# Kernel optimization log

Hardware: AMD Instinct MI355X
Metric: run time of the kernel (lower is better)

Reference implementation:

```python
import jax, jax.numpy as jnp
import numpy as np

EPS = 1e-10
WS = 5  # window_size
PAD = WS // 2


def _conv(x, k, pad_h, pad_w):
    # x: [N,1,H,W], k: [1,1,kh,kw], 'same'-style explicit padding
    return jax.lax.conv_general_dilated(
        x, k, window_strides=(1, 1),
        padding=[(pad_h, pad_h), (pad_w, pad_w)],
        dimension_numbers=("NCHW", "OIHW", "NCHW"))


def setup_inputs() -> dict:
    key = jax.random.key(0)
    B, C, Fr, T = 8, 2, 256, 2048
    spectrogram = jax.random.normal(key, (B, C, Fr, T), dtype=jnp.float32)
    # Gaussian kernel (window_size=5, sigma=1.0)
    c = WS // 2
    coords = jnp.arange(WS, dtype=jnp.float32) - c
    yy, xx = jnp.meshgrid(coords, coords, indexing="ij")
    g = jnp.exp(-(xx ** 2 + yy ** 2) / 2.0)
    gaussian_kernel = (g / g.sum()).reshape(1, 1, WS, WS)
    # Sobel kernels / 8
    sobel_x = (jnp.array([[-1, 0, 1], [-2, 0, 2], [-1, 0, 1]], jnp.float32) / 8.0).reshape(1, 1, 3, 3)
    sobel_y = (jnp.array([[-1, -2, -1], [0, 0, 0], [1, 2, 1]], jnp.float32) / 8.0).reshape(1, 1, 3, 3)
    # Harmonic kernel: 7x1 [-1,0,0,2,0,0,-1]
    hk = jnp.zeros(7, jnp.float32).at[0].set(-1.0).at[3].set(2.0).at[6].set(-1.0)
    harmonic_kernel = hk.reshape(1, 1, 7, 1)
    return {"spectrogram": spectrogram, "gaussian_kernel": gaussian_kernel,
            "sobel_x": sobel_x, "sobel_y": sobel_y, "harmonic_kernel": harmonic_kernel}


def _forward(spectrogram, gaussian_kernel, sobel_x, sobel_y, harmonic_kernel):
    B, C, Fr, T = spectrogram.shape
    # Per-channel 1-in/1-out convs == fold channels into batch.
    x = spectrogram.reshape(B * C, 1, Fr, T)

    grad_freq = _conv(x, sobel_y, 1, 1)
    grad_time = _conv(x, sobel_x, 1, 1)
    magnitude = jnp.sqrt(grad_freq ** 2 + grad_time ** 2 + EPS)
    angle = jnp.arctan2(grad_freq, grad_time + EPS)

    # ---- entropy (structure-tensor eigenvalue entropy) ----
    vx = magnitude * jnp.cos(angle)
    vy = magnitude * jnp.sin(angle)
    vxx = _conv(vx * vx, gaussian_kernel, PAD, PAD)
    vyy = _conv(vy * vy, gaussian_kernel, PAD, PAD)
    vxy = _conv(vx * vy, gaussian_kernel, PAD, PAD)
    trace = vxx + vyy
    det = vxx * vyy - vxy * vxy
    disc = jnp.sqrt(jnp.maximum(trace * trace - 4.0 * det, 0.0) + EPS)
    l1 = jnp.maximum((trace + disc) / 2.0, EPS)
    l2 = jnp.maximum((trace - disc) / 2.0, EPS)
    s = l1 + l2 + EPS
    p1, p2 = l1 / s, l2 / s
    entropy = -(p1 * jnp.log(p1 + EPS) + p2 * jnp.log(p2 + EPS)) / np.log(2.0)
    entropy = jnp.clip(entropy, 0.0, 1.0)

    # ---- alignment ----
    ux = jnp.cos(angle)
    uy = jnp.sin(angle)
    ux_avg = _conv(ux, gaussian_kernel, PAD, PAD)
    uy_avg = _conv(uy, gaussian_kernel, PAD, PAD)
    alignment = jnp.clip(jnp.sqrt(ux_avg ** 2 + uy_avg ** 2 + EPS), 0.0, 1.0)

    # ---- curvature ----
    dudx = _conv(ux, sobel_x, 1, 1)
    dudy = _conv(ux, sobel_y, 1, 1)
    dvdx = _conv(uy, sobel_x, 1, 1)
    dvdy = _conv(uy, sobel_y, 1, 1)
    curv = jnp.sqrt(dudx ** 2 + dudy ** 2 + dvdx ** 2 + dvdy ** 2 + EPS)
    curvature = _conv(curv, gaussian_kernel, PAD, PAD)

    # ---- harmonic coherence ----
    harm = jnp.abs(_conv(x, harmonic_kernel, 3, 0))
    local_energy = _conv(x ** 2, gaussian_kernel, PAD, PAD)
    harmonic = jnp.clip(harm / (local_energy + EPS), 0.0, 1.0)

    # ---- temporal stability: inverse temporal gradient magnitude, smoothed ----
    temporal = _conv(1.0 / (1.0 + jnp.abs(grad_time)), gaussian_kernel, PAD, PAD)
    temporal = jnp.clip(temporal, 0.0, 1.0)

    # ---- spectral flow: smoothed frequency-gradient magnitude ----
    spectral = jnp.clip(_conv(jnp.abs(grad_freq), gaussian_kernel, PAD, PAD), 0.0, 1.0)

    def chan_mean(f):  # [B*C,1,F,T] -> [B,1,F,T]
        return f.reshape(B, C, Fr, T).mean(axis=1, keepdims=True)

    return (chan_mean(entropy), chan_mean(alignment), chan_mean(curvature),
            chan_mean(harmonic), chan_mean(temporal), chan_mean(spectral))


def reference(spectrogram, gaussian_kernel, sobel_x, sobel_y, harmonic_kernel):
    return _forward(spectrogram, gaussian_kernel, sobel_x, sobel_y, harmonic_kernel)
```

## Files before the change

kernel.cpp:

```cpp
#include <hip/hip_runtime.h>
#include <hip/hip_fp16.h>


#define F_DIM 256
#define T_DIM 2048
#define B_DIM 8
#define C_DIM 2
#define TILE  32

#define XROWS 40
#define XS    40
#define UROWS 38
#define US    40
#define FROWS 36
#define FS    36
#define FH2   18
#define EPSF  1e-10f

template<bool V> struct BoolC { static constexpr bool value = V; };

static __device__ __forceinline__ __half2 pack_h2(float a, float b) {
    auto v = __builtin_amdgcn_cvt_pkrtz(a, b);
    return *(__half2*)&v;
}
static __device__ __forceinline__ float clamp01(float x) {
    return fminf(fmaxf(x, 0.f), 1.f);
}

__global__ __launch_bounds__(256, 4)
void audio_struct_fused(const float* __restrict__ x_in,
                        const float* __restrict__ gk_in,
                        float* __restrict__ out)
{
    __shared__ __align__(16) float   s_x [XROWS*XS];
    __shared__ __align__(16) __half2 s_u [UROWS*US];
    __shared__ __align__(16) __half2 s_P0[FROWS*FS];
    __shared__ __align__(16) __half2 s_P1[FROWS*FS];
    __shared__ __align__(16) __half2 s_P2[FROWS*FS];
    __shared__ __align__(16) float   s_tmp[TILE*FS];

    const int tx  = threadIdx.x;
    const int ty  = threadIdx.y;
    const int tid = ty * 32 + tx;
    const int t0  = blockIdx.x * TILE;
    const int f0  = blockIdx.y * TILE;
    const int b   = blockIdx.z;

    float r0 = gk_in[10], r1 = gk_in[11], r2 = gk_in[12], r3 = gk_in[13], r4 = gk_in[14];
    float winv = __builtin_amdgcn_rcpf(r0 + r1 + r2 + r3 + r4);
    const float w[5] = {r0*winv, r1*winv, r2*winv, r3*winv, r4*winv};
    const __half2 wh2[5] = {pack_h2(w[0],w[0]), pack_h2(w[1],w[1]), pack_h2(w[2],w[2]),
                            pack_h2(w[3],w[3]), pack_h2(w[4],w[4])};
    const __half2 h2z    = pack_h2(0.f, 0.f);
    const __half2 two    = pack_h2(2.f, 2.f);
    const __half2 eighth = pack_h2(0.125f, 0.125f);

    auto vpass_pair = [&](const __half2* src, __half2* dst) {
        const uint2* s = (const uint2*)src;
        uint2* d = (uint2*)dst;
        for (int idx = tid; idx < TILE * FH2; idx += 256) {
            __half2 a0 = h2z, a1 = h2z;
            #pragma unroll
            for (int i = 0; i < 5; ++i) {
                uint2 v = s[idx + i * FH2];
                a0 = __hfma2(wh2[i], *(const __half2*)&v.x, a0);
                a1 = __hfma2(wh2[i], *(const __half2*)&v.y, a1);
            }
            uint2 o; o.x = *(const unsigned*)&a0; o.y = *(const unsigned*)&a1;
            d[idx] = o;
        }
    };

    float acc[6][4];
    #pragma unroll
    for (int k = 0; k < 6; ++k)
        #pragma unroll
        for (int s = 0; s < 4; ++s) acc[k][s] = 0.0f;

    const bool interior = (f0 >= 4) && (f0 + TILE + 4 <= F_DIM) &&
                          (t0 >= 4) && (t0 + TILE + 4 <= T_DIM);

    auto phaseABC = [&](const float* xp, auto FASTC) {
        constexpr bool FAST = decltype(FASTC)::value;

        for (int idx = tid; idx < XROWS * 20; idx += 256) {
            int r  = idx / 20, c2 = idx - r * 20;
            float2 v;
            if (FAST) {
                v = *(const float2*)(xp + (size_t)(f0 + r - 4) * T_DIM + (t0 + c2 * 2 - 4));
            } else {
                int gf = f0 + r - 4;
                int gt = t0 + c2 * 2 - 4;
                v = make_float2(0.f, 0.f);
                if ((unsigned)gf < (unsigned)F_DIM && (unsigned)gt < (unsigned)T_DIM)
                    v = *(const float2*)(xp + (size_t)gf * T_DIM + gt);
            }
            *(float2*)&s_x[r * XS + c2 * 2] = v;
        }
        __syncthreads();

        for (int idx = tid; idx < UROWS * UROWS; idx += 256) {
            int r = idx / UROWS, cc = idx - r * UROWS;
            float ux = 0.f, uy = 0.f, trp = 0.f, dfp = 0.f, sxy = 0.f,
                  tin = 0.f, sf = 0.f;
            bool ok = true;
            if (!FAST) {
                int gfr = f0 + r - 3, gtc = t0 + cc - 3;
                ok = ((unsigned)gfr < (unsigned)F_DIM) & ((unsigned)gtc < (unsigned)T_DIM);
            }
            if (ok) {
                const float* xc = &s_x[(r + 1) * XS + (cc + 1)];
                float x00 = xc[-XS-1], x01 = xc[-XS], x02 = xc[-XS+1];
                float x10 = xc[-1],                   x12 = xc[1];
                float x20 = xc[XS-1],  x21 = xc[XS],  x22 = xc[XS+1];
                float gfv = ((x20 + 2.f*x21 + x22) - (x00 + 2.f*x01 + x02)) * 0.125f;
                float gtv = ((x02 + 2.f*x12 + x22) - (x00 + 2.f*x10 + x20)) * 0.125f;
                float gte = gtv + EPSF;
                float g2f = gfv * gfv;
                float d2  = fmaf(gte, gte, g2f);
                float rh  = __builtin_amdgcn_rsqf(d2);
                ux = gte * rh;
                uy = gfv * rh;
                float m2 = fmaf(gtv, gtv, g2f) + EPSF;
                trp = m2;
                dfp = m2 * (ux - uy) * (ux + uy);
                sxy = m2 * ux * uy;
                tin = __builtin_amdgcn_rcpf(1.0f + fabsf(gtv));
                sf  = fabsf(gfv);
            }
            s_u[r * US + cc + 1] = pack_h2(ux, uy);
            if (r >= 1 && r < UROWS - 1 && cc >= 1 && cc < UROWS - 1) {
                int fi = (r - 1) * FS + (cc - 1);
                s_P0[fi] = pack_h2(trp, dfp);
                s_P1[fi] = pack_h2(sxy, tin);
                s_P2[fi] = pack_h2(sf, 0.f);
            }
        }
        __syncthreads();

        for (int idx = tid; idx < FROWS * FROWS; idx += 256) {
            int r = idx / FROWS, cc = idx - r * FROWS;
            const __half2* up = &s_u[r * US + cc + 1];
            __half2 u00 = up[0],      u01 = up[1],      u02 = up[2];
            __half2 u10 = up[US],                       u12 = up[US+2];
            __half2 u20 = up[2*US],   u21 = up[2*US+1], u22 = up[2*US+2];
            __half2 l0 = __hadd2(u00, u20); l0 = __hfma2(two, u10, l0);
            __half2 l2 = __hadd2(u02, u22); l2 = __hfma2(two, u12, l2);
            __half2 dxv = __hmul2(__hsub2(l2, l0), eighth);
            __half2 t0h = __hadd2(u00, u02); t0h = __hfma2(two, u01, t0h);
            __half2 t2h = __hadd2(u20, u22); t2h = __hfma2(two, u21, t2h);
            __half2 dyv = __hmul2(__hsub2(t2h, t0h), eighth);
            float2 fx = __half22float2(dxv);
            float2 fy = __half22float2(dyv);
            float cv = __builtin_amdgcn_sqrtf(
                fmaf(fx.x, fx.x, fmaf(fx.y, fx.y,
                fmaf(fy.x, fy.x, fy.y * fy.y))) + EPSF);
            if (!FAST) {
                int gfr = f0 + r - 2, gtc = t0 + cc - 2;
                if (!(((unsigned)gfr < (unsigned)F_DIM) &
                      ((unsigned)gtc < (unsigned)T_DIM))) cv = 0.f;
            }
            ((__half*)s_P2)[2 * (r * FS + cc) + 1] = __float2half_rn(cv);
        }
        __syncthreads();
    };

    for (int c = 0; c < C_DIM; ++c) {
        __syncthreads();

        const float* xp = x_in + (size_t)(b * C_DIM + c) * F_DIM * T_DIM;
        if (interior) phaseABC(xp, BoolC<true>{});
        else          phaseABC(xp, BoolC<false>{});

        float trace_s[4], diff_s[4];
        __half2* tmp_h2 = (__half2*)s_tmp;

        vpass_pair(s_P0, tmp_h2);
        __syncthreads();

        #pragma unroll
        for (int s = 0; s < 4; ++s) {
            int ry = ty + 8 * s;
            float a = 0.f, bv = 0.f;
            #pragma unroll
            for (int j = 0; j < 5; ++j) {
                float2 v = __half22float2(tmp_h2[ry * FS + tx + j]);
                a += w[j] * v.x; bv += w[j] * v.y;
            }
            trace_s[s] = a; diff_s[s] = bv;
        }
        vpass_pair(s_P1, s_P0);
        __syncthreads();

        #pragma unroll
        for (int s = 0; s < 4; ++s) {
            int ry = ty + 8 * s;
            __half2 a = h2z;
            #pragma unroll
            for (int j = 0; j < 5; ++j)
                a = __hfma2(wh2[j], s_P0[ry * FS + tx + j], a);
            float2 v = __half22float2(a);
            float trace = trace_s[s], diff = diff_s[s];
            float disc  = __builtin_amdgcn_sqrtf(
                              fmaxf(diff * diff + 4.f * v.x * v.x, 0.f) + EPSF);
            float l1 = fmaxf(0.5f * (trace + disc), EPSF);
            float l2 = fmaxf(0.5f * (trace - disc), EPSF);
            float inv = __builtin_amdgcn_rcpf(l1 + l2 + EPSF);
            float p1 = l1 * inv, p2 = l2 * inv;
            float ent = -(p1 * __builtin_amdgcn_logf(p1 + EPSF)
                        + p2 * __builtin_amdgcn_logf(p2 + EPSF));
            acc[0][s] += 0.5f * clamp01(ent);
            acc[4][s] += 0.5f * clamp01(v.y);
        }
        vpass_pair(s_P2, tmp_h2);
        __syncthreads();

        #pragma unroll
        for (int s = 0; s < 4; ++s) {
            int ry = ty + 8 * s;
            __half2 a = h2z;
            #pragma unroll
            for (int j = 0; j < 5; ++j)
                a = __hfma2(wh2[j], tmp_h2[ry * FS + tx + j], a);
            float2 v = __half22float2(a);
            acc[5][s] += 0.5f * clamp01(v.x);
            acc[2][s] += 0.5f * v.y;
        }
        {
            const uint2* su2 = (const uint2*)s_u;
            uint2* dP1 = (uint2*)s_P1;
            for (int idx = tid; idx < TILE * FH2; idx += 256) {
                int r = idx / FH2, p = idx - r * FH2;
                const uint2* sp = su2 + (r + 1) * (US/2) + 1 + p;
                __half2 a0 = h2z, a1 = h2z;
                #pragma unroll
                for (int i = 0; i < 5; ++i) {
                    uint2 v = sp[i * (US/2)];
                    a0 = __hfma2(wh2[i], *(const __half2*)&v.x, a0);
                    a1 = __hfma2(wh2[i], *(const __half2*)&v.y, a1);
                }
                uint2 o; o.x = *(const unsigned*)&a0; o.y = *(const unsigned*)&a1;
                dP1[idx] = o;
            }
        }
        __syncthreads();

        #pragma unroll
        for (int s = 0; s < 4; ++s) {
            int ry = ty + 8 * s;
            __half2 a = h2z;
            #pragma unroll
            for (int j = 0; j < 5; ++j)
                a = __hfma2(wh2[j], s_P1[ry * FS + tx + j], a);
            float2 v = __half22float2(a);
            acc[1][s] += 0.5f * clamp01(
                __builtin_amdgcn_sqrtf(v.x * v.x + v.y * v.y + EPSF));
        }
        {
            const float2* sx2 = (const float2*)s_x;
            float2* dt2 = (float2*)s_tmp;
            for (int idx = tid; idx < TILE * FH2; idx += 256) {
                int r = idx / FH2, p = idx - r * FH2;
                const float2* sp = sx2 + (r + 2) * (XS/2) + 1 + p;
                float a = 0.f, bv = 0.f;
                #pragma unroll
                for (int i = 0; i < 5; ++i) {
                    float2 v = sp[i * (XS/2)];
                    a  = fmaf(w[i], v.x * v.x, a);
                    bv = fmaf(w[i], v.y * v.y, bv);
                }
                dt2[idx] = make_float2(a, bv);
            }
        }
        __syncthreads();

        #pragma unroll
        for (int s = 0; s < 4; ++s) {
            int ry = ty + 8 * s;
            float le = 0.f;
            #pragma unroll
            for (int j = 0; j < 5; ++j)
                le += w[j] * s_tmp[ry * FS + tx + j];
            float xm  = s_x[(ry + 1) * XS + tx + 4];
            float x0v = s_x[(ry + 4) * XS + tx + 4];
            float xpv = s_x[(ry + 7) * XS + tx + 4];
            float harm = fabsf(2.f * x0v - xm - xpv);
            acc[3][s] += 0.5f * clamp01(harm * __builtin_amdgcn_rcpf(le + EPSF));
        }
    }

    const size_t plane = (size_t)B_DIM * F_DIM * T_DIM;
    const size_t base  = (size_t)b * F_DIM * T_DIM + (size_t)f0 * T_DIM + t0 + tx;
    #pragma unroll
    for (int k = 0; k < 6; ++k)
        #pragma unroll
        for (int s = 0; s < 4; ++s)
            out[k * plane + base + (size_t)(ty + 8 * s) * T_DIM] = acc[k][s];
}

extern "C" void kernel_launch(void* const* d_in, const int* in_sizes, int n_in,
                              void* d_out, int out_size, void* d_ws, size_t ws_size,
                              hipStream_t stream) {
    const float* x  = (const float*)d_in[0];
    const float* gk = (const float*)d_in[1];
    float* out = (float*)d_out;
    dim3 grid(T_DIM / TILE, F_DIM / TILE, B_DIM);
    dim3 block(32, 8);
    audio_struct_fused<<<grid, block, 0, stream>>>(x, gk, out);
}
```

Before: 222.5 us.

## Prefetch next channel tile into registers and fold first vertical pass into phase

Global loads of the input tile now go into registers. They are issued early, before the filter weight setup for channel 0, and for channel 1 right after channel 0's tile is stored to shared memory, so their latency overlaps compute. The first vertical Gaussian pass is also moved inside the phase lambda, which removes one barrier. This adds 8 VGPRs of prefetch state, which could reduce occupancy under the 256x4 launch bound.

New measurement: 264.7 us. 1.19x slower.

```diff
diff --git a/kernel.cpp b/kernel.cpp
--- a/kernel.cpp
+++ b/kernel.cpp
@@ -16,6 +16,7 @@
 #define FS    36
 #define FH2   18
 #define EPSF  1e-10f
+#define NLD   4
 
 template<bool V> struct BoolC { static constexpr bool value = V; };
 
@@ -46,6 +47,50 @@
     const int f0  = blockIdx.y * TILE;
     const int b   = blockIdx.z;
 
+    const bool interior = (f0 >= 4) && (f0 + TILE + 4 <= F_DIM) &&
+                          (t0 >= 4) && (t0 + TILE + 4 <= T_DIM);
+
+    auto ld_tile = [&](const float* xp, float2* pf) {
+        if (interior) {
+            #pragma unroll
+            for (int k = 0; k < NLD; ++k) {
+                int idx = tid + k * 256;
+                if (idx < XROWS * 20) {
+                    int r = idx / 20, c2 = idx - r * 20;
+                    pf[k] = *(const float2*)(xp + (size_t)(f0 + r - 4) * T_DIM
+                                                + (t0 + c2 * 2 - 4));
+                }
+            }
+        } else {
+            #pragma unroll
+            for (int k = 0; k < NLD; ++k) {
+                int idx = tid + k * 256;
+                pf[k] = make_float2(0.f, 0.f);
+                if (idx < XROWS * 20) {
+                    int r = idx / 20, c2 = idx - r * 20;
+                    int gf = f0 + r - 4, gt = t0 + c2 * 2 - 4;
+                    if ((unsigned)gf < (unsigned)F_DIM && (unsigned)gt < (unsigned)T_DIM)
+                        pf[k] = *(const float2*)(xp + (size_t)gf * T_DIM + gt);
+                }
+            }
+        }
+    };
+    auto st_tile = [&](const float2* pf) {
+        #pragma unroll
+        for (int k = 0; k < NLD; ++k) {
+            int idx = tid + k * 256;
+            if (idx < XROWS * 20) {
+                int r = idx / 20, c2 = idx - r * 20;
+                *(float2*)&s_x[r * XS + c2 * 2] = pf[k];
+            }
+        }
+    };
+
+    const float* xp0 = x_in + (size_t)(b * C_DIM + 0) * F_DIM * T_DIM;
+    const float* xp1 = x_in + (size_t)(b * C_DIM + 1) * F_DIM * T_DIM;
+    float2 pf[NLD];
+    ld_tile(xp0, pf);
+
     float r0 = gk_in[10], r1 = gk_in[11], r2 = gk_in[12], r3 = gk_in[13], r4 = gk_in[14];
     float winv = __builtin_amdgcn_rcpf(r0 + r1 + r2 + r3 + r4);
     const float w[5] = {r0*winv, r1*winv, r2*winv, r3*winv, r4*winv};
@@ -77,27 +122,8 @@
         #pragma unroll
         for (int s = 0; s < 4; ++s) acc[k][s] = 0.0f;
 
-    const bool interior = (f0 >= 4) && (f0 + TILE + 4 <= F_DIM) &&
-                          (t0 >= 4) && (t0 + TILE + 4 <= T_DIM);
-
-    auto phaseABC = [&](const float* xp, auto FASTC) {
+    auto phaseBCD1 = [&](auto FASTC) {
         constexpr bool FAST = decltype(FASTC)::value;
-
-        for (int idx = tid; idx < XROWS * 20; idx += 256) {
-            int r  = idx / 20, c2 = idx - r * 20;
-            float2 v;
-            if (FAST) {
-                v = *(const float2*)(xp + (size_t)(f0 + r - 4) * T_DIM + (t0 + c2 * 2 - 4));
-            } else {
-                int gf = f0 + r - 4;
-                int gt = t0 + c2 * 2 - 4;
-                v = make_float2(0.f, 0.f);
-                if ((unsigned)gf < (unsigned)F_DIM && (unsigned)gt < (unsigned)T_DIM)
-                    v = *(const float2*)(xp + (size_t)gf * T_DIM + gt);
-            }
-            *(float2*)&s_x[r * XS + c2 * 2] = v;
-        }
-        __syncthreads();
 
         for (int idx = tid; idx < UROWS * UROWS; idx += 256) {
             int r = idx / UROWS, cc = idx - r * UROWS;
@@ -162,21 +188,22 @@
             }
             ((__half*)s_P2)[2 * (r * FS + cc) + 1] = __float2half_rn(cv);
         }
+        vpass_pair(s_P0, (__half2*)s_tmp);
         __syncthreads();
     };
 
     for (int c = 0; c < C_DIM; ++c) {
-        __syncthreads();
-
-        const float* xp = x_in + (size_t)(b * C_DIM + c) * F_DIM * T_DIM;
-        if (interior) phaseABC(xp, BoolC<true>{});
-        else          phaseABC(xp, BoolC<false>{});
+        if (c) __syncthreads();
+
+        st_tile(pf);
+        __syncthreads();
+        if (c == 0) ld_tile(xp1, pf);
+
+        if (interior) phaseBCD1(BoolC<true>{});
+        else          phaseBCD1(BoolC<false>{});
 
         float trace_s[4], diff_s[4];
         __half2* tmp_h2 = (__half2*)s_tmp;
-
-        vpass_pair(s_P0, tmp_h2);
-        __syncthreads();
 
         #pragma unroll
         for (int s = 0; s < 4; ++s) {
```
